# Optimization experiments

Hardware: AMD Instinct MI355X
Metric: run time of the kernel (lower is better)

Reference implementation:

```python
import jax, jax.numpy as jnp
import numpy as np

B, IN, HID, OUT, E, C, TOPK = 4096, 1024, 2048, 1024, 8, 1000, 2
EPS = 1e-6


def setup_inputs() -> dict:
    key = jax.random.key(0)
    ks = jax.random.split(key, 8)
    def xavier(k, fan_out, fan_in):
        lim = float(np.sqrt(6.0 / (fan_in + fan_out)))
        return jax.random.uniform(k, (fan_out, fan_in), jnp.float32, -lim, lim)
    return {
        "x": jax.random.normal(ks[0], (B, IN), jnp.float32),
        "Wg": xavier(ks[1], E, IN),
        "bg": jnp.zeros((E,), jnp.float32),
        "gamma": jnp.ones((1, E), jnp.float32),
        "beta": jnp.zeros((1, E), jnp.float32),
        "W1": xavier(ks[2], HID * E, IN),
        "b1": jnp.zeros((HID * E,), jnp.float32),
        "W2": xavier(ks[3], OUT * E, HID * E),
        "b2": jnp.zeros((OUT * E,), jnp.float32),
        "Wc": xavier(ks[4], C, OUT),
        "bc": jnp.zeros((C,), jnp.float32),
    }


def reference(x, Wg, bg, gamma, beta, W1, b1, W2, b2, Wc, bc):
    # gating (noise_std=0 -> no noise)
    gate_logits = x @ Wg.T + bg                      # [B, E]
    # GRN over expert dim
    Gx = jnp.linalg.norm(gate_logits, axis=1, keepdims=True)   # [B, 1]
    Nx = Gx / (jnp.mean(Gx, axis=0, keepdims=True) + EPS)      # [B, 1]
    gate_logits = gamma * (gate_logits * Nx) + beta
    gate_probs = jax.nn.softmax(gate_logits, axis=-1)
    topk_probs, topk_idx = jax.lax.top_k(gate_probs, TOPK)     # [B, K]
    # dense all-expert MLP (fc2 mixes across ALL experts' hidden units, as in source)
    h = jax.nn.relu(x @ W1.T + b1)                   # [B, HID*E]
    eo = (h @ W2.T + b2).reshape(B, E, OUT)          # [B, E, OUT]
    sel = jnp.take_along_axis(eo, topk_idx[:, :, None], axis=1)  # [B, K, OUT]
    out = jnp.einsum('bk,bkd->bd', topk_probs, sel)  # [B, OUT]
    return out @ Wc.T + bc                           # [B, C]
```

## Files before the change

### kernel.cpp

```cpp
#include <hip/hip_runtime.h>
#include <stdint.h>

#define B_SZ   4096
#define IN_SZ  1024
#define NE     8
#define NC     1000
#define HIDE   16384
#define OUTE   1024
#define GEPS   1e-6f
#define NSPLIT 2
#define KSPL   8192

typedef __attribute__((ext_vector_type(8))) short short8;
typedef __attribute__((ext_vector_type(4))) float floatx4;

__device__ __forceinline__ unsigned short f2bf(float f) {
    unsigned u = __float_as_uint(f);
    u += 0x7fffu + ((u >> 16) & 1u);
    return (unsigned short)(u >> 16);
}
__device__ __forceinline__ float bf2f(unsigned short h) {
    return __uint_as_float(((unsigned)h) << 16);
}

__device__ __forceinline__ void async16(const void* g, void* l) {
    __builtin_amdgcn_global_load_lds(
        (const __attribute__((address_space(1))) void*)g,
        (__attribute__((address_space(3))) void*)l, 16, 0, 0);
}

__global__ __launch_bounds__(256) void k_cvt(const float* __restrict__ src,
                                             unsigned short* __restrict__ dst, int n) {
    int i = (blockIdx.x * 256 + threadIdx.x) * 4;
    int stride = gridDim.x * 256 * 4;
    for (; i < n; i += stride) {
        float4 v = *(const float4*)(src + i);
        ushort4 o;
        o.x = f2bf(v.x); o.y = f2bf(v.y); o.z = f2bf(v.z); o.w = f2bf(v.w);
        *(ushort4*)(dst + i) = o;
    }
}

__global__ __launch_bounds__(256) void k_gate(const float* __restrict__ x,
                                              const float* __restrict__ Wg,
                                              const float* __restrict__ bg,
                                              float* __restrict__ logits,
                                              float* __restrict__ Gx) {
    int wid = threadIdx.x >> 6, lane = threadIdx.x & 63;
    int b = blockIdx.x * 4 + wid;
    const float* xr = x + (size_t)b * IN_SZ;
    float xv[16];
#pragma unroll
    for (int t = 0; t < 16; ++t) xv[t] = xr[lane + 64 * t];
    float lg[NE];
#pragma unroll
    for (int e = 0; e < NE; ++e) {
        const float* wr = Wg + e * IN_SZ;
        float s = 0.f;
#pragma unroll
        for (int t = 0; t < 16; ++t) s += xv[t] * wr[lane + 64 * t];
#pragma unroll
        for (int m = 32; m >= 1; m >>= 1) s += __shfl_xor(s, m, 64);
        lg[e] = s + bg[e];
    }
    if (lane == 0) {
        float ss = 0.f;
#pragma unroll
        for (int e = 0; e < NE; ++e) { logits[b * NE + e] = lg[e]; ss += lg[e] * lg[e]; }
        Gx[b] = sqrtf(ss);
    }
}

__global__ __launch_bounds__(1024) void k_gsum(const float* __restrict__ Gx, float* __restrict__ gsum) {
    __shared__ float sm[1024];
    int t = threadIdx.x;
    sm[t] = Gx[t] + Gx[t + 1024] + Gx[t + 2048] + Gx[t + 3072];
    __syncthreads();
    for (int m = 512; m >= 1; m >>= 1) {
        if (t < m) sm[t] += sm[t + m];
        __syncthreads();
    }
    if (t == 0) gsum[0] = sm[0];
}

__global__ void k_zeroctrl(int* ctrl) {
    if (threadIdx.x < 24) ctrl[threadIdx.x] = 0;
}

__global__ __launch_bounds__(256) void k_topk(const float* __restrict__ logits,
                                              const float* __restrict__ Gx,
                                              const float* __restrict__ gsum,
                                              const float* __restrict__ gamma,
                                              const float* __restrict__ beta,
                                              int* __restrict__ tidx, float* __restrict__ tp,
                                              int* __restrict__ counts) {
    int b = blockIdx.x * 256 + threadIdx.x;
    float nx = Gx[b] / (gsum[0] * (1.0f / (float)B_SZ) + GEPS);
    float l[NE];
    float mx = -1e30f;
#pragma unroll
    for (int e = 0; e < NE; ++e) {
        l[e] = gamma[e] * (logits[b * NE + e] * nx) + beta[e];
        mx = fmaxf(mx, l[e]);
    }
    float se = 0.f;
#pragma unroll
    for (int e = 0; e < NE; ++e) { l[e] = expf(l[e] - mx); se += l[e]; }
    float inv = 1.f / se;
    int i0 = 0; float p0 = l[0];
#pragma unroll
    for (int e = 1; e < NE; ++e) if (l[e] > p0) { p0 = l[e]; i0 = e; }
    int i1 = -1; float p1 = -1.f;
#pragma unroll
    for (int e = 0; e < NE; ++e) if (e != i0 && l[e] > p1) { p1 = l[e]; i1 = e; }
    tidx[b * 2 + 0] = i0; tidx[b * 2 + 1] = i1;
    tp[b * 2 + 0] = p0 * inv; tp[b * 2 + 1] = p1 * inv;
    atomicAdd(&counts[i0], 1);
    atomicAdd(&counts[i1], 1);
}

__global__ void k_offsets(const int* __restrict__ counts, int* __restrict__ offs) {
    if (threadIdx.x == 0) {
        int a = 0;
        for (int e = 0; e < NE; ++e) { offs[e] = a; a += counts[e]; }
    }
}

__global__ __launch_bounds__(256) void k_fill(const int* __restrict__ tidx, const float* __restrict__ tp,
                                              const int* __restrict__ offs, int* __restrict__ cursors,
                                              int* __restrict__ rowsw, int* __restrict__ slotof) {
    int b = blockIdx.x * 256 + threadIdx.x;
#pragma unroll
    for (int k = 0; k < 2; ++k) {
        int e = tidx[b * 2 + k];
        int pos = atomicAdd(&cursors[e], 1);
        int at = offs[e] + pos;
        rowsw[at] = b * 2 + k;
        slotof[b * 2 + k] = at;
    }
}


__device__ __forceinline__ void core64(
    const unsigned short* pa0, const unsigned short* pa1,
    const unsigned short* pa2, const unsigned short* pa3,
    const unsigned short* pb0, const unsigned short* pb1,
    const unsigned short* pb2, const unsigned short* pb3,
    short* sA, short* sB, int nkt, int wm, int wn, int tid, int lane,
    floatx4 acc[4][4])
{
    char* sAc = (char*)sA;
    char* sBc = (char*)sB;
    const int sl = ((lane >> 4) ^ (lane & 7)) * 8;
    int aoff[4], boff[4];
#pragma unroll
    for (int i = 0; i < 4; ++i) {
        aoff[i] = (wm * 64 + i * 16 + (lane & 15)) * 64 + sl;
        boff[i] = (wn * 64 + i * 16 + (lane & 15)) * 64 + sl;
    }
    for (int kt = 0; kt < nkt; ++kt) {
        __syncthreads();
        async16(pa0, sAc + tid * 16);
        async16(pa1, sAc + 4096 + tid * 16);
        async16(pa2, sAc + 8192 + tid * 16);
        async16(pa3, sAc + 12288 + tid * 16);
        async16(pb0, sBc + tid * 16);
        async16(pb1, sBc + 4096 + tid * 16);
        async16(pb2, sBc + 8192 + tid * 16);
        async16(pb3, sBc + 12288 + tid * 16);
        pa0 += 64; pa1 += 64; pa2 += 64; pa3 += 64;
        pb0 += 64; pb1 += 64; pb2 += 64; pb3 += 64;
        __syncthreads();
        short8 a0[4], a1[4], b0[4], b1[4];
#pragma unroll
        for (int i = 0; i < 4; ++i) {
            a0[i] = *(const short8*)(sA + aoff[i]);
            a1[i] = *(const short8*)(sA + (aoff[i] ^ 32));
            b0[i] = *(const short8*)(sB + boff[i]);
            b1[i] = *(const short8*)(sB + (boff[i] ^ 32));
        }
#pragma unroll
        for (int i = 0; i < 4; ++i)
#pragma unroll
            for (int j = 0; j < 4; ++j) {
                acc[i][j] = __builtin_amdgcn_mfma_f32_16x16x32_bf16(a0[i], b0[j], acc[i][j], 0, 0, 0);
                acc[i][j] = __builtin_amdgcn_mfma_f32_16x16x32_bf16(a1[i], b1[j], acc[i][j], 0, 0, 0);
            }
    }
}

__global__ __launch_bounds__(256) void k_h8(const unsigned short* __restrict__ xb,
                                            const unsigned short* __restrict__ w1b,
                                            const float* __restrict__ b1,
                                            unsigned short* __restrict__ hout) {
    __shared__ __align__(16) short sA[128 * 64];
    __shared__ __align__(16) short sB[128 * 64];
    const int tid = threadIdx.x, lane = tid & 63, wid = tid >> 6;
    const int wm = wid >> 1, wn = wid & 1;
    const int wg = (blockIdx.x & 7) * (gridDim.x >> 3) + (blockIdx.x >> 3);
    const int mt = wg & 31, nt = wg >> 5;
    const int m0 = mt * 128, n0 = nt * 128;
    const int srow = tid >> 3;
    const int cswz = ((tid & 7) ^ (srow & 7)) * 8;
    const unsigned short* pa[4];
    const unsigned short* pb[4];
#pragma unroll
    for (int c = 0; c < 4; ++c) {
        pa[c] = xb  + (size_t)(m0 + 32 * c + srow) * IN_SZ + cswz;
        pb[c] = w1b + (size_t)(n0 + 32 * c + srow) * IN_SZ + cswz;
    }
    floatx4 acc[4][4] = {};
    core64(pa[0], pa[1], pa[2], pa[3], pb[0], pb[1], pb[2], pb[3],
           sA, sB, IN_SZ / 64, wm, wn, tid, lane, acc);
#pragma unroll
    for (int i = 0; i < 4; ++i)
#pragma unroll
        for (int j = 0; j < 4; ++j)
#pragma unroll
            for (int r = 0; r < 4; ++r) {
                int row = m0 + wm * 64 + i * 16 + (lane >> 4) * 4 + r;
                int col = n0 + wn * 64 + j * 16 + (lane & 15);
                float v = acc[i][j][r] + b1[col];
                hout[(size_t)row * HIDE + col] = f2bf(fmaxf(v, 0.f));
            }
}

__global__ __launch_bounds__(256) void k_moe(const unsigned short* __restrict__ h,
                                             const unsigned short* __restrict__ w2b,
                                             const int* __restrict__ counts,
                                             const int* __restrict__ offs,
                                             const int* __restrict__ rowsw,
                                             unsigned short* __restrict__ parts) {
    const int wg = (blockIdx.x & 7) * (gridDim.x >> 3) + (blockIdx.x >> 3);
    const int mt = wg & 31, nt = (wg >> 5) & 7, sp = (wg >> 8) & 1, e = wg >> 9;
    const int gn = counts[e];
    if (mt * 128 >= gn) return;
    const int gbase = offs[e];
    __shared__ __align__(16) short sA[128 * 64];
    __shared__ __align__(16) short sB[128 * 64];
    const int tid = threadIdx.x, lane = tid & 63, wid = tid >> 6;
    const int wm = wid >> 1, wn = wid & 1;
    const int srow = tid >> 3;
    const int cswz = ((tid & 7) ^ (srow & 7)) * 8;
    const unsigned short* pa[4];
    const unsigned short* pb[4];
#pragma unroll
    for (int c = 0; c < 4; ++c) {
        int lr = mt * 128 + 32 * c + srow;
        if (lr > gn - 1) lr = gn - 1;
        int grow = rowsw[gbase + lr] >> 1;
        pa[c] = h + (size_t)grow * HIDE + sp * KSPL + cswz;
        pb[c] = w2b + (size_t)(e * OUTE + nt * 128 + 32 * c + srow) * HIDE + sp * KSPL + cswz;
    }
    floatx4 acc[4][4] = {};
    core64(pa[0], pa[1], pa[2], pa[3], pb[0], pb[1], pb[2], pb[3],
           sA, sB, KSPL / 64, wm, wn, tid, lane, acc);
    unsigned short* pbase = parts + (size_t)sp * B_SZ * 2 * OUTE;
#pragma unroll
    for (int i = 0; i < 4; ++i)
#pragma unroll
        for (int j = 0; j < 4; ++j)
#pragma unroll
            for (int r = 0; r < 4; ++r) {
                int lr = mt * 128 + wm * 64 + i * 16 + (lane >> 4) * 4 + r;
                if (lr < gn) {
                    int at = gbase + lr;
                    int col = nt * 128 + wn * 64 + j * 16 + (lane & 15);
                    pbase[(size_t)at * OUTE + col] = f2bf(acc[i][j][r]);
                }
            }
}

__global__ __launch_bounds__(256) void k_reduce(const unsigned short* __restrict__ parts,
                                                const int* __restrict__ slotof,
                                                const int* __restrict__ tidx,
                                                const float* __restrict__ tp,
                                                const float* __restrict__ b2,
                                                unsigned short* __restrict__ ymix) {
    int i = blockIdx.x * 256 + threadIdx.x;
    int b = i >> 8, col = (i & 255) * 4;
    int at0 = slotof[b * 2], at1 = slotof[b * 2 + 1];
    int e0 = tidx[b * 2], e1 = tidx[b * 2 + 1];
    float q0 = tp[b * 2], q1 = tp[b * 2 + 1];
    float y0[4] = {0.f, 0.f, 0.f, 0.f}, y1[4] = {0.f, 0.f, 0.f, 0.f};
#pragma unroll
    for (int sp = 0; sp < NSPLIT; ++sp) {
        ushort4 u0 = *(const ushort4*)(parts + ((size_t)sp * B_SZ * 2 + at0) * OUTE + col);
        ushort4 u1 = *(const ushort4*)(parts + ((size_t)sp * B_SZ * 2 + at1) * OUTE + col);
        y0[0] += bf2f(u0.x); y0[1] += bf2f(u0.y); y0[2] += bf2f(u0.z); y0[3] += bf2f(u0.w);
        y1[0] += bf2f(u1.x); y1[1] += bf2f(u1.y); y1[2] += bf2f(u1.z); y1[3] += bf2f(u1.w);
    }
    float4 bb0 = *(const float4*)(b2 + (size_t)e0 * OUTE + col);
    float4 bb1 = *(const float4*)(b2 + (size_t)e1 * OUTE + col);
    ushort4 o;
    o.x = f2bf(q0 * (y0[0] + bb0.x) + q1 * (y1[0] + bb1.x));
    o.y = f2bf(q0 * (y0[1] + bb0.y) + q1 * (y1[1] + bb1.y));
    o.z = f2bf(q0 * (y0[2] + bb0.z) + q1 * (y1[2] + bb1.z));
    o.w = f2bf(q0 * (y0[3] + bb0.w) + q1 * (y1[3] + bb1.w));
    *(ushort4*)(ymix + (size_t)b * OUTE + col) = o;
}

__device__ __forceinline__ void gemm_core(const unsigned short* sa0, const unsigned short* sa1,
                                          const unsigned short* sb0, const unsigned short* sb1,
                                          short* sA, short* sB, int nkt, int wid, int lane,
                                          floatx4 acc[4][4]) {
    short* ldsA0 = sA + (wid * 2 + 0) * 512;
    short* ldsA1 = sA + (wid * 2 + 1) * 512;
    short* ldsB0 = sB + (wid * 2 + 0) * 512;
    short* ldsB1 = sB + (wid * 2 + 1) * 512;
    const int wm = wid >> 1, wn = wid & 1;
    int aoff[4], boff[4];
#pragma unroll
    for (int i = 0; i < 4; ++i) {
        aoff[i] = (wm * 64 + i * 16 + (lane & 15)) * 32 + (lane >> 4) * 8;
        boff[i] = (wn * 64 + i * 16 + (lane & 15)) * 32 + (lane >> 4) * 8;
    }
    for (int kt = 0; kt < nkt; ++kt) {
        __syncthreads();
        async16(sa0, ldsA0);
        async16(sa1, ldsA1);
        async16(sb0, ldsB0);
        async16(sb1, ldsB1);
        sa0 += 32; sa1 += 32; sb0 += 32; sb1 += 32;
        __syncthreads();
        short8 av[4], bv[4];
#pragma unroll
        for (int i = 0; i < 4; ++i) av[i] = *(const short8*)(sA + aoff[i]);
#pragma unroll
        for (int j = 0; j < 4; ++j) bv[j] = *(const short8*)(sB + boff[j]);
#pragma unroll
        for (int i = 0; i < 4; ++i)
#pragma unroll
            for (int j = 0; j < 4; ++j)
                acc[i][j] = __builtin_amdgcn_mfma_f32_16x16x32_bf16(av[i], bv[j], acc[i][j], 0, 0, 0);
    }
}

__global__ __launch_bounds__(256) void k_gemm_out(const unsigned short* __restrict__ ymix,
                                                  const unsigned short* __restrict__ wcb,
                                                  const float* __restrict__ bc,
                                                  float* __restrict__ out) {
    const int mt = blockIdx.x >> 3, nt = blockIdx.x & 7;
    const int m0 = mt * 128, n0 = nt * 128;
    __shared__ __align__(16) short sA[128 * 32];
    __shared__ __align__(16) short sB[128 * 32];
    const int lane = threadIdx.x & 63, wid = threadIdx.x >> 6;
    const int t0row = (wid * 2 + 0) * 16 + (lane >> 2);
    const int t1row = (wid * 2 + 1) * 16 + (lane >> 2);
    const int kb = (lane & 3) * 8;
    int br0 = n0 + t0row; if (br0 > NC - 1) br0 = NC - 1;
    int br1 = n0 + t1row; if (br1 > NC - 1) br1 = NC - 1;
    const unsigned short* sa0 = ymix + (size_t)(m0 + t0row) * IN_SZ + kb;
    const unsigned short* sa1 = ymix + (size_t)(m0 + t1row) * IN_SZ + kb;
    const unsigned short* sb0 = wcb + (size_t)br0 * IN_SZ + kb;
    const unsigned short* sb1 = wcb + (size_t)br1 * IN_SZ + kb;
    floatx4 acc[4][4] = {};
    gemm_core(sa0, sa1, sb0, sb1, sA, sB, IN_SZ / 32, wid, lane, acc);
    const int wm = wid >> 1, wn = wid & 1;
#pragma unroll
    for (int i = 0; i < 4; ++i)
#pragma unroll
        for (int j = 0; j < 4; ++j)
#pragma unroll
            for (int r = 0; r < 4; ++r) {
                int row = m0 + wm * 64 + i * 16 + (lane >> 4) * 4 + r;
                int col = n0 + wn * 64 + j * 16 + (lane & 15);
                if (col < NC)
                    out[(size_t)row * NC + col] = acc[i][j][r] + bc[col];
            }
}

extern "C" void kernel_launch(void* const* d_in, const int* in_sizes, int n_in,
                              void* d_out, int out_size, void* d_ws, size_t ws_size,
                              hipStream_t stream) {
    const float* x     = (const float*)d_in[0];
    const float* Wg    = (const float*)d_in[1];
    const float* bg    = (const float*)d_in[2];
    const float* gamma = (const float*)d_in[3];
    const float* beta  = (const float*)d_in[4];
    const float* W1    = (const float*)d_in[5];
    const float* b1    = (const float*)d_in[6];
    const float* W2    = (const float*)d_in[7];
    const float* b2    = (const float*)d_in[8];
    const float* Wc    = (const float*)d_in[9];
    const float* bc    = (const float*)d_in[10];
    float* out = (float*)d_out;

    char* ws = (char*)d_ws;
    size_t o = 0;
    auto carve = [&](size_t bytes) { char* p = ws + o; o += (bytes + 255) & ~(size_t)255; return p; };
    unsigned short* xb    = (unsigned short*)carve((size_t)B_SZ * IN_SZ * 2);
    unsigned short* w1b   = (unsigned short*)carve((size_t)HIDE * IN_SZ * 2);
    unsigned short* w2b   = (unsigned short*)carve((size_t)NE * OUTE * HIDE * 2);
    unsigned short* wcb   = (unsigned short*)carve((size_t)NC * IN_SZ * 2);
    unsigned short* h     = (unsigned short*)carve((size_t)B_SZ * HIDE * 2);
    unsigned short* parts = (unsigned short*)carve((size_t)NSPLIT * B_SZ * 2 * OUTE * 2);
    unsigned short* ymix  = (unsigned short*)carve((size_t)B_SZ * OUTE * 2);
    float* logits = (float*)carve((size_t)B_SZ * NE * 4);
    float* Gx     = (float*)carve((size_t)B_SZ * 4);
    int*   tidx   = (int*)carve((size_t)B_SZ * 2 * 4);
    float* tp     = (float*)carve((size_t)B_SZ * 2 * 4);
    int*   rowsw  = (int*)carve((size_t)B_SZ * 2 * 4);
    int*   slotof = (int*)carve((size_t)B_SZ * 2 * 4);
    int*   ctrl   = (int*)carve(256);
    int* counts  = ctrl;
    int* cursors = ctrl + 8;
    int* offs    = ctrl + 16;
    float* gsum  = (float*)(ctrl + 24);

    k_cvt<<<2048, 256, 0, stream>>>(x,  xb,  B_SZ * IN_SZ);
    k_cvt<<<2048, 256, 0, stream>>>(W1, w1b, HIDE * IN_SZ);
    k_cvt<<<2048, 256, 0, stream>>>(W2, w2b, NE * OUTE * HIDE);
    k_cvt<<<2048, 256, 0, stream>>>(Wc, wcb, NC * IN_SZ);

    k_gate<<<B_SZ / 4, 256, 0, stream>>>(x, Wg, bg, logits, Gx);
    k_gsum<<<1, 1024, 0, stream>>>(Gx, gsum);
    k_zeroctrl<<<1, 64, 0, stream>>>(ctrl);
    k_topk<<<B_SZ / 256, 256, 0, stream>>>(logits, Gx, gsum, gamma, beta, tidx, tp, counts);
    k_offsets<<<1, 64, 0, stream>>>(counts, offs);
    k_fill<<<B_SZ / 256, 256, 0, stream>>>(tidx, tp, offs, cursors, rowsw, slotof);

    k_h8<<<(B_SZ / 128) * (HIDE / 128), 256, 0, stream>>>(xb, w1b, b1, h);
    k_moe<<<NE * 32 * 8 * NSPLIT, 256, 0, stream>>>(h, w2b, counts, offs, rowsw, parts);
    k_reduce<<<B_SZ, 256, 0, stream>>>(parts, slotof, tidx, tp, b2, ymix);
    k_gemm_out<<<(B_SZ / 128) * 8, 256, 0, stream>>>(ymix, wcb, bc, out);
}
```

Baseline: 1.063 ms.

## Double-buffer LDS tiles in GEMM cores and unify output GEMM onto shared core

Replaces the single-buffered GEMM main loop with a two-stage LDS ping-pong, so the async global-to-LDS copies for the next K tile are issued while MFMAs run on the current one. It also adds a priority bump around the MFMA block. The output-projection GEMM moves from its BK=32 core onto the same swizzled BK=64 double-buffered core. The cost is 64 KB of dynamic shared memory per block, which can reduce occupancy. Each buffer is overwritten only after the barrier that follows its compute, though the async-copy completion ordering before each read relies on that barrier alone.

```diff
diff --git a/kernel.cpp b/kernel.cpp
--- a/kernel.cpp
+++ b/kernel.cpp
@@ -141,16 +141,47 @@
 }
 
 
-__device__ __forceinline__ void core64(
-    const unsigned short* pa0, const unsigned short* pa1,
-    const unsigned short* pa2, const unsigned short* pa3,
-    const unsigned short* pb0, const unsigned short* pb1,
-    const unsigned short* pb2, const unsigned short* pb3,
-    short* sA, short* sB, int nkt, int wm, int wn, int tid, int lane,
-    floatx4 acc[4][4])
-{
-    char* sAc = (char*)sA;
-    char* sBc = (char*)sB;
+__device__ __forceinline__ void stage_bk64(const unsigned short* const* pa,
+                                           const unsigned short* const* pb,
+                                           char* bufc, int koff, int tid) {
+#pragma unroll
+    for (int c = 0; c < 4; ++c) {
+        async16(pa[c] + koff, bufc + c * 4096 + tid * 16);
+        async16(pb[c] + koff, bufc + 16384 + c * 4096 + tid * 16);
+    }
+}
+
+__device__ __forceinline__ void compute_bk64(const short* buf, const int* aoff, const int* boff,
+                                             floatx4 acc[4][4]) {
+    const short* sA = buf;
+    const short* sB = buf + 8192;
+    short8 a0[4], a1[4], b0[4], b1[4];
+#pragma unroll
+    for (int i = 0; i < 4; ++i) {
+        a0[i] = *(const short8*)(sA + aoff[i]);
+        a1[i] = *(const short8*)(sA + (aoff[i] ^ 32));
+        b0[i] = *(const short8*)(sB + boff[i]);
+        b1[i] = *(const short8*)(sB + (boff[i] ^ 32));
+    }
+    asm volatile("s_waitcnt lgkmcnt(0)" ::: "memory");
+    __builtin_amdgcn_sched_barrier(0);
+    __builtin_amdgcn_s_setprio(1);
+#pragma unroll
+    for (int i = 0; i < 4; ++i)
+#pragma unroll
+        for (int j = 0; j < 4; ++j) {
+            acc[i][j] = __builtin_amdgcn_mfma_f32_16x16x32_bf16(a0[i], b0[j], acc[i][j], 0, 0, 0);
+            acc[i][j] = __builtin_amdgcn_mfma_f32_16x16x32_bf16(a1[i], b1[j], acc[i][j], 0, 0, 0);
+        }
+    __builtin_amdgcn_s_setprio(0);
+}
+
+__device__ __forceinline__ void core64db(const unsigned short* const* pa,
+                                         const unsigned short* const* pb,
+                                         short* smem, int nkt, int wm, int wn,
+                                         int tid, int lane, floatx4 acc[4][4]) {
+    char* b0c = (char*)smem;
+    char* b1c = b0c + 32768;
     const int sl = ((lane >> 4) ^ (lane & 7)) * 8;
     int aoff[4], boff[4];
 #pragma unroll
@@ -158,34 +189,16 @@
         aoff[i] = (wm * 64 + i * 16 + (lane & 15)) * 64 + sl;
         boff[i] = (wn * 64 + i * 16 + (lane & 15)) * 64 + sl;
     }
-    for (int kt = 0; kt < nkt; ++kt) {
+    stage_bk64(pa, pb, b0c, 0, tid);
+    __syncthreads();
+#pragma unroll 1
+    for (int kt = 0; kt < nkt; kt += 2) {
+        if (kt + 1 < nkt) stage_bk64(pa, pb, b1c, (kt + 1) * 64, tid);
+        compute_bk64(smem, aoff, boff, acc);
         __syncthreads();
-        async16(pa0, sAc + tid * 16);
-        async16(pa1, sAc + 4096 + tid * 16);
-        async16(pa2, sAc + 8192 + tid * 16);
-        async16(pa3, sAc + 12288 + tid * 16);
-        async16(pb0, sBc + tid * 16);
-        async16(pb1, sBc + 4096 + tid * 16);
-        async16(pb2, sBc + 8192 + tid * 16);
-        async16(pb3, sBc + 12288 + tid * 16);
-        pa0 += 64; pa1 += 64; pa2 += 64; pa3 += 64;
-        pb0 += 64; pb1 += 64; pb2 += 64; pb3 += 64;
+        if (kt + 2 < nkt) stage_bk64(pa, pb, b0c, (kt + 2) * 64, tid);
+        compute_bk64(smem + 16384, aoff, boff, acc);
         __syncthreads();
-        short8 a0[4], a1[4], b0[4], b1[4];
-#pragma unroll
-        for (int i = 0; i < 4; ++i) {
-            a0[i] = *(const short8*)(sA + aoff[i]);
-            a1[i] = *(const short8*)(sA + (aoff[i] ^ 32));
-            b0[i] = *(const short8*)(sB + boff[i]);
-            b1[i] = *(const short8*)(sB + (boff[i] ^ 32));
-        }
-#pragma unroll
-        for (int i = 0; i < 4; ++i)
-#pragma unroll
-            for (int j = 0; j < 4; ++j) {
-                acc[i][j] = __builtin_amdgcn_mfma_f32_16x16x32_bf16(a0[i], b0[j], acc[i][j], 0, 0, 0);
-                acc[i][j] = __builtin_amdgcn_mfma_f32_16x16x32_bf16(a1[i], b1[j], acc[i][j], 0, 0, 0);
-            }
     }
 }
 
@@ -193,8 +206,7 @@
                                             const unsigned short* __restrict__ w1b,
                                             const float* __restrict__ b1,
                                             unsigned short* __restrict__ hout) {
-    __shared__ __align__(16) short sA[128 * 64];
-    __shared__ __align__(16) short sB[128 * 64];
+    extern __shared__ short smem[];
     const int tid = threadIdx.x, lane = tid & 63, wid = tid >> 6;
     const int wm = wid >> 1, wn = wid & 1;
     const int wg = (blockIdx.x & 7) * (gridDim.x >> 3) + (blockIdx.x >> 3);
@@ -210,8 +222,7 @@
         pb[c] = w1b + (size_t)(n0 + 32 * c + srow) * IN_SZ + cswz;
     }
     floatx4 acc[4][4] = {};
-    core64(pa[0], pa[1], pa[2], pa[3], pb[0], pb[1], pb[2], pb[3],
-           sA, sB, IN_SZ / 64, wm, wn, tid, lane, acc);
+    core64db(pa, pb, smem, IN_SZ / 64, wm, wn, tid, lane, acc);
 #pragma unroll
     for (int i = 0; i < 4; ++i)
 #pragma unroll
@@ -236,8 +247,7 @@
     const int gn = counts[e];
     if (mt * 128 >= gn) return;
     const int gbase = offs[e];
-    __shared__ __align__(16) short sA[128 * 64];
-    __shared__ __align__(16) short sB[128 * 64];
+    extern __shared__ short smem[];
     const int tid = threadIdx.x, lane = tid & 63, wid = tid >> 6;
     const int wm = wid >> 1, wn = wid & 1;
     const int srow = tid >> 3;
@@ -253,8 +263,7 @@
         pb[c] = w2b + (size_t)(e * OUTE + nt * 128 + 32 * c + srow) * HIDE + sp * KSPL + cswz;
     }
     floatx4 acc[4][4] = {};
-    core64(pa[0], pa[1], pa[2], pa[3], pb[0], pb[1], pb[2], pb[3],
-           sA, sB, KSPL / 64, wm, wn, tid, lane, acc);
+    core64db(pa, pb, smem, KSPL / 64, wm, wn, tid, lane, acc);
     unsigned short* pbase = parts + (size_t)sp * B_SZ * 2 * OUTE;
 #pragma unroll
     for (int i = 0; i < 4; ++i)
@@ -300,63 +309,27 @@
     *(ushort4*)(ymix + (size_t)b * OUTE + col) = o;
 }
 
-__device__ __forceinline__ void gemm_core(const unsigned short* sa0, const unsigned short* sa1,
-                                          const unsigned short* sb0, const unsigned short* sb1,
-                                          short* sA, short* sB, int nkt, int wid, int lane,
-                                          floatx4 acc[4][4]) {
-    short* ldsA0 = sA + (wid * 2 + 0) * 512;
-    short* ldsA1 = sA + (wid * 2 + 1) * 512;
-    short* ldsB0 = sB + (wid * 2 + 0) * 512;
-    short* ldsB1 = sB + (wid * 2 + 1) * 512;
-    const int wm = wid >> 1, wn = wid & 1;
-    int aoff[4], boff[4];
-#pragma unroll
-    for (int i = 0; i < 4; ++i) {
-        aoff[i] = (wm * 64 + i * 16 + (lane & 15)) * 32 + (lane >> 4) * 8;
-        boff[i] = (wn * 64 + i * 16 + (lane & 15)) * 32 + (lane >> 4) * 8;
-    }
-    for (int kt = 0; kt < nkt; ++kt) {
-        __syncthreads();
-        async16(sa0, ldsA0);
-        async16(sa1, ldsA1);
-        async16(sb0, ldsB0);
-        async16(sb1, ldsB1);
-        sa0 += 32; sa1 += 32; sb0 += 32; sb1 += 32;
-        __syncthreads();
-        short8 av[4], bv[4];
-#pragma unroll
-        for (int i = 0; i < 4; ++i) av[i] = *(const short8*)(sA + aoff[i]);
-#pragma unroll
-        for (int j = 0; j < 4; ++j) bv[j] = *(const short8*)(sB + boff[j]);
-#pragma unroll
-        for (int i = 0; i < 4; ++i)
-#pragma unroll
-            for (int j = 0; j < 4; ++j)
-                acc[i][j] = __builtin_amdgcn_mfma_f32_16x16x32_bf16(av[i], bv[j], acc[i][j], 0, 0, 0);
-    }
-}
-
 __global__ __launch_bounds__(256) void k_gemm_out(const unsigned short* __restrict__ ymix,
                                                   const unsigned short* __restrict__ wcb,
                                                   const float* __restrict__ bc,
                                                   float* __restrict__ out) {
     const int mt = blockIdx.x >> 3, nt = blockIdx.x & 7;
     const int m0 = mt * 128, n0 = nt * 128;
-    __shared__ __align__(16) short sA[128 * 32];
-    __shared__ __align__(16) short sB[128 * 32];
-    const int lane = threadIdx.x & 63, wid = threadIdx.x >> 6;
-    const int t0row = (wid * 2 + 0) * 16 + (lane >> 2);
-    const int t1row = (wid * 2 + 1) * 16 + (lane >> 2);
-    const int kb = (lane & 3) * 8;
-    int br0 = n0 + t0row; if (br0 > NC - 1) br0 = NC - 1;
-    int br1 = n0 + t1row; if (br1 > NC - 1) br1 = NC - 1;
-    const unsigned short* sa0 = ymix + (size_t)(m0 + t0row) * IN_SZ + kb;
-    const unsigned short* sa1 = ymix + (size_t)(m0 + t1row) * IN_SZ + kb;
-    const unsigned short* sb0 = wcb + (size_t)br0 * IN_SZ + kb;
-    const unsigned short* sb1 = wcb + (size_t)br1 * IN_SZ + kb;
+    extern __shared__ short smem[];
+    const int tid = threadIdx.x, lane = tid & 63, wid = tid >> 6;
+    const int wm = wid >> 1, wn = wid & 1;
+    const int srow = tid >> 3;
+    const int cswz = ((tid & 7) ^ (srow & 7)) * 8;
+    const unsigned short* pa[4];
+    const unsigned short* pb[4];
+#pragma unroll
+    for (int c = 0; c < 4; ++c) {
+        pa[c] = ymix + (size_t)(m0 + 32 * c + srow) * IN_SZ + cswz;
+        int br = n0 + 32 * c + srow; if (br > NC - 1) br = NC - 1;
+        pb[c] = wcb + (size_t)br * IN_SZ + cswz;
+    }
     floatx4 acc[4][4] = {};
-    gemm_core(sa0, sa1, sb0, sb1, sA, sB, IN_SZ / 32, wid, lane, acc);
-    const int wm = wid >> 1, wn = wid & 1;
+    core64db(pa, pb, smem, IN_SZ / 64, wm, wn, tid, lane, acc);
 #pragma unroll
     for (int i = 0; i < 4; ++i)
 #pragma unroll
@@ -408,6 +381,10 @@
     int* offs    = ctrl + 16;
     float* gsum  = (float*)(ctrl + 24);
 
+    hipFuncSetAttribute((const void*)k_h8,       hipFuncAttributeMaxDynamicSharedMemorySize, 65536);
+    hipFuncSetAttribute((const void*)k_moe,      hipFuncAttributeMaxDynamicSharedMemorySize, 65536);
+    hipFuncSetAttribute((const void*)k_gemm_out, hipFuncAttributeMaxDynamicSharedMemorySize, 65536);
+
     k_cvt<<<2048, 256, 0, stream>>>(x,  xb,  B_SZ * IN_SZ);
     k_cvt<<<2048, 256, 0, stream>>>(W1, w1b, HIDE * IN_SZ);
     k_cvt<<<2048, 256, 0, stream>>>(W2, w2b, NE * OUTE * HIDE);
@@ -420,8 +397,8 @@
     k_offsets<<<1, 64, 0, stream>>>(counts, offs);
     k_fill<<<B_SZ / 256, 256, 0, stream>>>(tidx, tp, offs, cursors, rowsw, slotof);
 
-    k_h8<<<(B_SZ / 128) * (HIDE / 128), 256, 0, stream>>>(xb, w1b, b1, h);
-    k_moe<<<NE * 32 * 8 * NSPLIT, 256, 0, stream>>>(h, w2b, counts, offs, rowsw, parts);
+    k_h8<<<(B_SZ / 128) * (HIDE / 128), 256, 65536, stream>>>(xb, w1b, b1, h);
+    k_moe<<<NE * 32 * 8 * NSPLIT, 256, 65536, stream>>>(h, w2b, counts, offs, rowsw, parts);
     k_reduce<<<B_SZ, 256, 0, stream>>>(parts, slotof, tidx, tp, b2, ymix);
-    k_gemm_out<<<(B_SZ / 128) * 8, 256, 0, stream>>>(ymix, wcb, bc, out);
-}
+    k_gemm_out<<<(B_SZ / 128) * 8, 256, 65536, stream>>>(ymix, wcb, bc, out);
+}
```

Measured after the change: 922.4 us. 13.3% less time.
